# Optimization experiments

Hardware: AMD Instinct MI355X
Metric: run time of the kernel (lower is better)

## Reference

```python
import jax, jax.numpy as jnp
import numpy as np

TILE = 16


def _quat_to_rotmat(q):
    # q: [N,4] (r,x,y,z), normalized first (torch.nn.functional.normalize semantics)
    q = q / jnp.linalg.norm(q, axis=-1, keepdims=True)
    r, x, y, z = q[:, 0], q[:, 1], q[:, 2], q[:, 3]
    R = jnp.stack([
        1 - 2 * (y * y + z * z), 2 * (x * y - r * z), 2 * (x * z + r * y),
        2 * (x * y + r * z), 1 - 2 * (x * x + z * z), 2 * (y * z - r * x),
        2 * (x * z - r * y), 2 * (y * z + r * x), 1 - 2 * (x * x + y * y),
    ], axis=-1).reshape(-1, 3, 3)
    return R


def _forward(xyz, scaling, rotation, opacity, rot, res):
    N = xyz.shape[0]
    xy_mean = xyz[:, :2] * (res / 2.0)                      # [N,2]

    # cov2d: L = R @ diag(raw scaling); cov3d = L L^T; S = diag(W,H,0)
    R = _quat_to_rotmat(rotation)                            # [N,3,3]
    L = R * scaling[:, None, :]                              # [N,3,3]
    cov3d = L @ jnp.swapaxes(L, 1, 2)                        # [N,3,3]
    S = jnp.diag(jnp.array([res, res, 0.0], dtype=xyz.dtype))
    A = S @ rot                                              # [3,3]
    cov2d = jnp.einsum('ij,njk,lk->nil', A, cov3d, A)[:, :2, :2]  # [N,2,2]
    c00, c01 = cov2d[:, 0, 0], cov2d[:, 0, 1]
    c10, c11 = cov2d[:, 1, 0], cov2d[:, 1, 1]

    # radius = ceil(3 * sqrt(max eigenvalue)) with standard 3DGS clamp
    det = c00 * c11 - c01 * c10
    mid = 0.5 * (c00 + c11)
    sq = jnp.sqrt(jnp.maximum(mid * mid - det, 0.1))
    radii = jnp.ceil(3.0 * jnp.sqrt(jnp.maximum(mid + sq, mid - sq)))  # [N]

    # rect (torch-splatting get_rect): clip corners to [0, res-1]
    rmin = jnp.clip(xy_mean - radii[:, None], 0.0, res - 1.0)          # [N,2]
    rmax = jnp.clip(xy_mean + radii[:, None], 0.0, res - 1.0)

    # tile/gaussian overlap mask (replicates the python double loop's in_mask)
    nt = res // TILE
    tstart = (jnp.arange(nt) * TILE).astype(xyz.dtype)                 # [nt]
    mask_x = jnp.minimum(rmax[None, :, 0], tstart[:, None] + TILE - 1) > \
             jnp.maximum(rmin[None, :, 0], tstart[:, None])            # [nt,N]
    mask_y = jnp.minimum(rmax[None, :, 1], tstart[:, None] + TILE - 1) > \
             jnp.maximum(rmin[None, :, 1], tstart[:, None])            # [nt,N]
    mask = mask_y[:, None, :] & mask_x[None, :, :]                     # [nt_h,nt_w,N]
    maskpix = jnp.repeat(jnp.repeat(mask, TILE, axis=0), TILE, axis=1)
    maskpix = maskpix.reshape(res * res, N).astype(xyz.dtype)          # [P,N]

    # pixel grid, meshgrid(x, y, indexing='xy'): pixel (i,j) -> (x[j], y[i])
    coords = jnp.linspace(-res / 2.0, res / 2.0 - 1.0, res, dtype=xyz.dtype) + 0.5
    px = jnp.tile(coords, res)      # [P] x varies fastest
    py = jnp.repeat(coords, res)    # [P]

    # conic = cov2d^{-1} (analytic 2x2 inverse)
    idet = 1.0 / det
    i00, i11 = c11 * idet, c00 * idet
    i01, i10 = -c01 * idet, -c10 * idet

    dx0 = px[:, None] - xy_mean[None, :, 0]                            # [P,N]
    dx1 = py[:, None] - xy_mean[None, :, 1]                            # [P,N]
    power = -0.5 * (dx0 * dx0 * i00 + dx1 * dx1 * i11 + dx0 * dx1 * (i01 + i10))
    w = jnp.exp(power)                                                 # [P,N]

    # alpha = sum_n w * raw_opacity, masked by tile overlap
    acc = jnp.einsum('pn,pn,n->p', w, maskpix, opacity[:, 0])
    return acc.reshape(res, res, 1)


def setup_inputs() -> dict:
    key = jax.random.key(0)
    k1, k2, k3, k4, k5 = jax.random.split(key, 5)
    N, res = 1024, 256
    return {
        'xyz': jax.random.uniform(k1, (N, 3), dtype=jnp.float32),
        'scaling': jax.random.uniform(k2, (N, 3), dtype=jnp.float32),
        'rotation': jax.random.normal(k3, (N, 4), dtype=jnp.float32),
        'opacity': jax.random.uniform(k4, (N, 1), dtype=jnp.float32),
        'rot': jax.random.normal(k5, (3, 3), dtype=jnp.float32),
        'res': res,
    }


def reference(xyz, scaling, rotation, opacity, rot, res):
    return _forward(xyz, scaling, rotation, opacity, rot, res)
```

## Files before the change

kernel.cpp:

```cpp
#include <hip/hip_runtime.h>
#include <math.h>


#define TILE 16
#define MAXG 1024
#define NW   8
#define GPW  (MAXG / NW)

__global__ __launch_bounds__(512, 1) void gs_fused(
    const float* __restrict__ xyz, const float* __restrict__ scaling,
    const float* __restrict__ rotation, const float* __restrict__ opacity,
    const float* __restrict__ rot, float* __restrict__ out,
    int N, int res, int nt)
{
    __shared__ float4 sP[MAXG];
    __shared__ float2 sQ[MAXG];
    __shared__ float4 sR[NW][64];

    const int tid = threadIdx.x;
    const int w = tid >> 6, l = tid & 63;
    const int tX = blockIdx.x % nt, tY = blockIdx.x / nt;
    const float resf = (float)res;

    const int px0 = tX * TILE + (l & 7) * 2;
    const int py0 = tY * TILE + (l >> 3) * 2;
    const float ctr = resf * 0.5f - 0.5f;
    const float Xa = (float)px0 - ctr, Xb = Xa + 1.f;
    const float Ya = (float)py0 - ctr, Yb = Ya + 1.f;
    const float Xa2 = Xa*Xa, Xb2 = Xb*Xb, Ya2 = Ya*Ya, Yb2 = Yb*Yb;
    const float XaYa = Xa*Ya, XbYa = Xb*Ya, XaYb = Xa*Yb, XbYb = Xb*Yb;

    const float tx0 = (float)(tX * TILE), tx1 = tx0 + (float)(TILE - 1);
    const float ty0 = (float)(tY * TILE), ty1 = ty0 + (float)(TILE - 1);

    float acc00 = 0.f, acc10 = 0.f, acc01 = 0.f, acc11 = 0.f;

    for (int base = 0; base < N; base += MAXG) {
        const int C = min(MAXG, N - base);

        #pragma unroll
        for (int k = 0; k < MAXG / 512; ++k) {
            int slot = tid + k * 512;
            float4 P = make_float4(0.f, 0.f, 0.f, 0.f);
            float2 Q = make_float2(0.f, -INFINITY);
            if (slot < C) {
                int n = base + slot;
                float qr = rotation[4*n+0], qx = rotation[4*n+1];
                float qy = rotation[4*n+2], qz = rotation[4*n+3];
                float inv = 1.0f / sqrtf(qr*qr + qx*qx + qy*qy + qz*qz);
                float r = qr*inv, x = qx*inv, y = qy*inv, z = qz*inv;

                float R00 = 1.f - 2.f*(y*y + z*z), R01 = 2.f*(x*y - r*z), R02 = 2.f*(x*z + r*y);
                float R10 = 2.f*(x*y + r*z), R11 = 1.f - 2.f*(x*x + z*z), R12 = 2.f*(y*z - r*x);
                float R20 = 2.f*(x*z - r*y), R21 = 2.f*(y*z + r*x), R22 = 1.f - 2.f*(x*x + y*y);

                float s0 = scaling[3*n+0], s1 = scaling[3*n+1], s2 = scaling[3*n+2];
                float L00 = R00*s0, L01 = R01*s1, L02 = R02*s2;
                float L10 = R10*s0, L11 = R11*s1, L12 = R12*s2;
                float L20 = R20*s0, L21 = R21*s1, L22 = R22*s2;

                float a00 = resf*rot[0], a01 = resf*rot[1], a02 = resf*rot[2];
                float a10 = resf*rot[3], a11 = resf*rot[4], a12 = resf*rot[5];
                float b00 = a00*L00 + a01*L10 + a02*L20;
                float b01 = a00*L01 + a01*L11 + a02*L21;
                float b02 = a00*L02 + a01*L12 + a02*L22;
                float b10 = a10*L00 + a11*L10 + a12*L20;
                float b11 = a10*L01 + a11*L11 + a12*L21;
                float b12 = a10*L02 + a11*L12 + a12*L22;
                float c00 = b00*b00 + b01*b01 + b02*b02;
                float c01 = b00*b10 + b01*b11 + b02*b12;
                float c11 = b10*b10 + b11*b11 + b12*b12;

                float det = c00*c11 - c01*c01;
                float mid = 0.5f*(c00 + c11);
                float sq  = sqrtf(fmaxf(mid*mid - det, 0.1f));
                float lam = fmaxf(mid + sq, mid - sq);
                float radii = ceilf(3.0f * sqrtf(lam));

                float mx = xyz[3*n+0] * (resf*0.5f);
                float my = xyz[3*n+1] * (resf*0.5f);
                float rminx = fminf(fmaxf(mx - radii, 0.f), resf - 1.f);
                float rmaxx = fminf(fmaxf(mx + radii, 0.f), resf - 1.f);
                float rminy = fminf(fmaxf(my - radii, 0.f), resf - 1.f);
                float rmaxy = fminf(fmaxf(my + radii, 0.f), resf - 1.f);

                bool pass = (fminf(rmaxx, tx1) > fmaxf(rminx, tx0)) &&
                            (fminf(rmaxy, ty1) > fmaxf(rminy, ty0));

                float idet = 1.0f / det;
                const float L2E = 1.44269504088896340736f;
                float A  = -0.5f * L2E * c11 * idet;
                float B  = -0.5f * L2E * c00 * idet;
                float Cc =         L2E * c01 * idet;

                float c3 = -2.f*A*mx - Cc*my;
                float c4 = -2.f*B*my - Cc*mx;
                float c5 = A*mx*mx + B*my*my + Cc*mx*my + log2f(opacity[n]);

                P = make_float4(A, B, Cc, c3);
                Q = make_float2(c4, pass ? c5 : -INFINITY);
            }
            sP[slot] = P;
            sQ[slot] = Q;
        }
        __syncthreads();

        const int g0 = w * GPW;
        #pragma unroll 4
        for (int i = g0; i < g0 + GPW; ++i) {
            float4 p  = sP[i];
            float2 qv = sQ[i];
            float ux_a = fmaf(p.x, Xa2, p.w * Xa);
            float ux_b = fmaf(p.x, Xb2, p.w * Xb);
            float vy_a = fmaf(p.y, Ya2, fmaf(qv.x, Ya, qv.y));
            float vy_b = fmaf(p.y, Yb2, fmaf(qv.x, Yb, qv.y));
            acc00 += __builtin_amdgcn_exp2f(fmaf(p.z, XaYa, ux_a + vy_a));
            acc10 += __builtin_amdgcn_exp2f(fmaf(p.z, XbYa, ux_b + vy_a));
            acc01 += __builtin_amdgcn_exp2f(fmaf(p.z, XaYb, ux_a + vy_b));
            acc11 += __builtin_amdgcn_exp2f(fmaf(p.z, XbYb, ux_b + vy_b));
        }
        __syncthreads();
    }

    sR[w][l] = make_float4(acc00, acc10, acc01, acc11);
    __syncthreads();
    if (w == 0) {
        float4 s = sR[0][l];
        #pragma unroll
        for (int k = 1; k < NW; ++k) {
            float4 t = sR[k][l];
            s.x += t.x; s.y += t.y; s.z += t.z; s.w += t.w;
        }
        float* o = out + py0 * res + px0;
        *(float2*)(o)       = make_float2(s.x, s.y);
        *(float2*)(o + res) = make_float2(s.z, s.w);
    }
}

extern "C" void kernel_launch(void* const* d_in, const int* in_sizes, int n_in,
                              void* d_out, int out_size, void* d_ws, size_t ws_size,
                              hipStream_t stream) {
    const float* xyz      = (const float*)d_in[0];
    const float* scaling  = (const float*)d_in[1];
    const float* rotation = (const float*)d_in[2];
    const float* opacity  = (const float*)d_in[3];
    const float* rot      = (const float*)d_in[4];
    int N   = in_sizes[0] / 3;
    int res = (int)(sqrt((double)out_size) + 0.5);
    int nt  = res / TILE;

    float* out = (float*)d_out;

    gs_fused<<<dim3(nt * nt), 512, 0, stream>>>(
        xyz, scaling, rotation, opacity, rot, out, N, res, nt);
}
```

Measured before the change: 20.51 us.

## Double block to 1024 threads and use finite-difference quadratic evaluation

The block grows from 8 to 16 waves, so each wave processes half as many gaussians per tile and the 1024 gaussian parameters are computed once per thread instead of twice. The inner loop now evaluates the quadratic exponent at the first pixel and reaches the other three of the 2x2 quad by adding forward differences, which needs fewer FMAs per gaussian. The trade-offs are the larger block, which may limit occupancy and add to the final cross-wave reduction, and the difference scheme, which can change float rounding slightly.

```diff
diff --git a/kernel.cpp b/kernel.cpp
--- a/kernel.cpp
+++ b/kernel.cpp
@@ -4,10 +4,10 @@
 
 #define TILE 16
 #define MAXG 1024
-#define NW   8
+#define NW   16
 #define GPW  (MAXG / NW)
 
-__global__ __launch_bounds__(512, 1) void gs_fused(
+__global__ __launch_bounds__(1024, 1) void gs_fused(
     const float* __restrict__ xyz, const float* __restrict__ scaling,
     const float* __restrict__ rotation, const float* __restrict__ opacity,
     const float* __restrict__ rot, float* __restrict__ out,
@@ -27,8 +27,9 @@
     const float ctr = resf * 0.5f - 0.5f;
     const float Xa = (float)px0 - ctr, Xb = Xa + 1.f;
     const float Ya = (float)py0 - ctr, Yb = Ya + 1.f;
-    const float Xa2 = Xa*Xa, Xb2 = Xb*Xb, Ya2 = Ya*Ya, Yb2 = Yb*Yb;
-    const float XaYa = Xa*Ya, XbYa = Xb*Ya, XaYb = Xa*Yb, XbYb = Xb*Yb;
+    const float XaYa = Xa * Ya;
+    const float sXab = Xa + Xb;
+    const float sYab = Ya + Yb;
 
     const float tx0 = (float)(tX * TILE), tx1 = tx0 + (float)(TILE - 1);
     const float ty0 = (float)(tY * TILE), ty1 = ty0 + (float)(TILE - 1);
@@ -38,9 +39,7 @@
     for (int base = 0; base < N; base += MAXG) {
         const int C = min(MAXG, N - base);
 
-        #pragma unroll
-        for (int k = 0; k < MAXG / 512; ++k) {
-            int slot = tid + k * 512;
+        for (int slot = tid; slot < MAXG; slot += 1024) {
             float4 P = make_float4(0.f, 0.f, 0.f, 0.f);
             float2 Q = make_float2(0.f, -INFINITY);
             if (slot < C) {
@@ -110,14 +109,22 @@
         for (int i = g0; i < g0 + GPW; ++i) {
             float4 p  = sP[i];
             float2 qv = sQ[i];
-            float ux_a = fmaf(p.x, Xa2, p.w * Xa);
-            float ux_b = fmaf(p.x, Xb2, p.w * Xb);
-            float vy_a = fmaf(p.y, Ya2, fmaf(qv.x, Ya, qv.y));
-            float vy_b = fmaf(p.y, Yb2, fmaf(qv.x, Yb, qv.y));
-            acc00 += __builtin_amdgcn_exp2f(fmaf(p.z, XaYa, ux_a + vy_a));
-            acc10 += __builtin_amdgcn_exp2f(fmaf(p.z, XbYa, ux_b + vy_a));
-            acc01 += __builtin_amdgcn_exp2f(fmaf(p.z, XaYb, ux_a + vy_b));
-            acc11 += __builtin_amdgcn_exp2f(fmaf(p.z, XbYb, ux_b + vy_b));
+            float t1  = fmaf(p.x, Xa, p.w);
+            float t3  = fmaf(p.y, Ya, qv.x);
+            float t2  = fmaf(t1, Xa, qv.y);
+            float t4  = fmaf(t3, Ya, t2);
+            float qaa = fmaf(p.z, XaYa, t4);
+            float dx0 = fmaf(p.x, sXab, p.w);
+            float dy0 = fmaf(p.y, sYab, qv.x);
+            float dX  = fmaf(p.z, Ya, dx0);
+            float dY  = fmaf(p.z, Xa, dy0);
+            float qba = qaa + dX;
+            float qab = qaa + dY;
+            float qbb = qab + (dX + p.z);
+            acc00 += __builtin_amdgcn_exp2f(qaa);
+            acc10 += __builtin_amdgcn_exp2f(qba);
+            acc01 += __builtin_amdgcn_exp2f(qab);
+            acc11 += __builtin_amdgcn_exp2f(qbb);
         }
         __syncthreads();
     }
@@ -151,6 +158,6 @@
 
     float* out = (float*)d_out;
 
-    gs_fused<<<dim3(nt * nt), 512, 0, stream>>>(
+    gs_fused<<<dim3(nt * nt), 1024, 0, stream>>>(
         xyz, scaling, rotation, opacity, rot, out, N, res, nt);
 }
```

Result: faster. 19.60 us (-4.4%).
